# Performance work log

Hardware: AMD Instinct MI355X
Metric: run time of the kernel (lower is better)

Reference implementation:

```python
import jax, jax.numpy as jnp
import numpy as np

EMBED = 2048
HEADS = 16


def setup_inputs() -> dict:
    key = jax.random.key(0)
    ks = jax.random.split(key, 9)
    N, L, E = 4, 2048, EMBED
    inp = {
        "query": jax.random.normal(ks[0], (N, L, E), dtype=jnp.float32),
        "keys": jax.random.normal(ks[1], (N, L, E), dtype=jnp.float32),
        "values": jax.random.normal(ks[2], (N, L, E), dtype=jnp.float32),
        "mask": jax.random.randint(ks[3], (N, L), 0, 2, dtype=jnp.int32),
        # nn.Linear weights, stored torch-style as (out_features, in_features)
        "Wq": jax.random.normal(ks[4], (E, E), dtype=jnp.float32) * (E ** -0.5),
        "Wk": jax.random.normal(ks[5], (E, E), dtype=jnp.float32) * (E ** -0.5),
        "Wv": jax.random.normal(ks[6], (E, E), dtype=jnp.float32) * (E ** -0.5),
        "Wo": jax.random.normal(ks[7], (E, E), dtype=jnp.float32) * (E ** -0.5),
        "bo": jax.random.normal(ks[8], (E,), dtype=jnp.float32) * 0.01,
    }
    return inp


def reference(query, keys, values, mask, Wq, Wk, Wv, Wo, bo):
    N, Lq, E = query.shape
    Lk = keys.shape[1]
    H = HEADS
    D = E // H
    # projections (torch Linear: y = x @ W.T)
    q = (query @ Wq.T).reshape(N, Lq, H, D)   # nqhd
    k = (keys @ Wk.T).reshape(N, Lk, H, D)    # nkhd
    v = (values @ Wv.T).reshape(N, Lk, H, D)  # nkhd
    # attention scores per head: (N, H, Lq, Lk)
    energy = jnp.einsum('nqhd,nkhd->nhqk', q, k)
    # 2D mask (N, Lk): 0 = masked out, broadcast over heads and query positions
    m = mask[:, None, None, :]
    energy = jnp.where(m == 0, jnp.float32(-1e20), energy)
    # source scales by sqrt(embed_size), not sqrt(head_dim)
    attn = jax.nn.softmax(energy * (E ** -0.5), axis=-1)
    out = jnp.einsum('nhqk,nkhd->nqhd', attn, v).reshape(N, Lq, E)
    return out @ Wo.T + bo
```

## Files before the change

kernel.cpp:

```cpp
#include <hip/hip_runtime.h>
#include <stdint.h>


typedef __bf16 bf16;
typedef __bf16 bf16x2 __attribute__((ext_vector_type(2)));
typedef __bf16 bf16x4 __attribute__((ext_vector_type(4)));
typedef __bf16 bf16x8 __attribute__((ext_vector_type(8)));
typedef float  f32x4  __attribute__((ext_vector_type(4)));
typedef uint32_t u32x4 __attribute__((ext_vector_type(4)));

#define MFMA16(a, b, c) __builtin_amdgcn_mfma_f32_16x16x32_bf16(a, b, c, 0, 0, 0)

__device__ __forceinline__ void gload_lds16(const void* g, void* s) {
  __builtin_amdgcn_global_load_lds(
      (const __attribute__((address_space(1))) void*)g,
      (__attribute__((address_space(3))) void*)s, 16, 0, 0);
}

__device__ __forceinline__ uint32_t pkbf(float a, float b) {
  return __builtin_bit_cast(uint32_t, (bf16x2){(bf16)a, (bf16)b});
}

__global__ __launch_bounds__(256) void cvt_bf16(const float* __restrict__ src,
                                                bf16* __restrict__ dst, long n) {
  long i = ((long)blockIdx.x * 256 + threadIdx.x) * 4;
  if (i < n) {
    f32x4 f = *(const f32x4*)(src + i);
    bf16x4 h = { (bf16)f.x, (bf16)f.y, (bf16)f.z, (bf16)f.w };
    *(bf16x4*)(dst + i) = h;
  }
}

__global__ __launch_bounds__(256) void gather_cvt(const float* __restrict__ src,
                                                  bf16* __restrict__ dst,
                                                  const int* __restrict__ idx) {
  long i = (long)blockIdx.x * 256 + threadIdx.x;
  int row = (int)(i >> 8);
  int u = (int)(i & 255);
  int n = row >> 11, p = row & 2047;
  long srow = ((long)n << 11) + idx[(n << 11) + p];
  const float* s = src + srow * 2048 + u * 8;
  f32x4 a = *(const f32x4*)s;
  f32x4 b = *(const f32x4*)(s + 4);
  bf16x8 h = { (bf16)a.x, (bf16)a.y, (bf16)a.z, (bf16)a.w,
               (bf16)b.x, (bf16)b.y, (bf16)b.z, (bf16)b.w };
  *(bf16x8*)(dst + (long)row * 2048 + u * 8) = h;
}

__global__ __launch_bounds__(256) void mask_compact(const int* __restrict__ mask,
                                                    int* __restrict__ idx,
                                                    int* __restrict__ cnts) {
  const int n = blockIdx.x;
  const int t = threadIdx.x, l = t & 63, w = t >> 6;
  const int* m = mask + n * 2048;
  __shared__ int wtot[4];
  int f[8], tt = 0;
  const int base = t * 8;
#pragma unroll
  for (int i = 0; i < 8; ++i) { f[i] = (m[base + i] != 0); tt += f[i]; }
  int sc = tt;
#pragma unroll
  for (int d = 1; d < 64; d <<= 1) {
    int v = __shfl_up(sc, d);
    if (l >= d) sc += v;
  }
  if (l == 63) wtot[w] = sc;
  __syncthreads();
  int woff = 0;
#pragma unroll
  for (int i = 0; i < 4; ++i) if (i < w) woff += wtot[i];
  int off = woff + sc - tt;
#pragma unroll
  for (int i = 0; i < 8; ++i)
    if (f[i]) { idx[n * 2048 + off] = base + i; ++off; }
  int total = wtot[0] + wtot[1] + wtot[2] + wtot[3];
  for (int p = total + t; p < 2048; p += 256) idx[n * 2048 + p] = 2047;
  if (t == 0) { cnts[n] = total; cnts[4 + n] = (total + 127) & ~127; }
}

template <int AEXIT, int OUT_F32, int ADD_BIAS>
__global__ __launch_bounds__(512, 2) void gemm256(const bf16* __restrict__ A,
                                                  const bf16* __restrict__ B,
                                                  void* __restrict__ Cout,
                                                  const float* __restrict__ bias,
                                                  const int* __restrict__ cnts) {
  constexpr int K = 2048, LDC = 2048, NT = 32;
  constexpr int TILE = 256 * 64;
  __shared__ bf16 S[2 * 2 * TILE];
  const int t = threadIdx.x;
  const int l = t & 63, w = t >> 6;
  const int wr = w >> 2, wc = w & 3;
  const int l15 = l & 15, l4 = l >> 4;

  const int Mb = ((blockIdx.x & 7) << 2) + (blockIdx.x >> 3);
  const long tm = (long)Mb * 256;
  const long tn = (long)blockIdx.y * 256;

  if constexpr (AEXIT) {
    int n = (int)(tm >> 11);
    if ((int)(tm & 2047) >= cnts[4 + n]) return;
  }

  const bf16* Ab = A + tm * K;
  const bf16* Bb = B + tn * K;

  auto stage = [&](int T, int p) {
    bf16* sA = S + p * 2 * TILE;
    bf16* sB = sA + TILE;
    const bf16* Ak = Ab + T * 64;
    const bf16* Bk = Bb + T * 64;
#pragma unroll
    for (int i = 0; i < 4; ++i) {
      int u = i * 512 + t;
      int row = u >> 3, slot = u & 7;
      int ss = slot ^ (row & 7);
      gload_lds16(Ak + (long)row * K + ss * 8, sA + u * 8);
    }
#pragma unroll
    for (int i = 0; i < 4; ++i) {
      int u = i * 512 + t;
      int row = u >> 3, slot = u & 7;
      int ss = slot ^ (row & 7);
      gload_lds16(Bk + (long)row * K + ss * 8, sB + u * 8);
    }
  };

  f32x4 acc[8][4];
#pragma unroll
  for (int i = 0; i < 8; ++i)
#pragma unroll
    for (int j = 0; j < 4; ++j) acc[i][j] = (f32x4){0.f, 0.f, 0.f, 0.f};

  stage(0, 0);

  for (int T = 0; T < NT; ++T) {
    const int p = T & 1;
    const bf16* sA = S + p * 2 * TILE;
    const bf16* sB = sA + TILE;

    asm volatile("" ::: "memory");
    __builtin_amdgcn_s_barrier();
    asm volatile("" ::: "memory");
    if (T + 1 < NT) {
      stage(T + 1, p ^ 1);
      asm volatile("s_waitcnt vmcnt(8)" ::: "memory");
    } else {
      asm volatile("s_waitcnt vmcnt(0)" ::: "memory");
    }
    __builtin_amdgcn_s_barrier();
    asm volatile("" ::: "memory");

#pragma unroll
    for (int kk = 0; kk < 2; ++kk) {
      bf16x8 af[8], bf[4];
#pragma unroll
      for (int mi = 0; mi < 8; ++mi) {
        int row = wr * 128 + mi * 16 + l15;
        int slot = (kk * 4 + l4) ^ (row & 7);
        af[mi] = *(const bf16x8*)(sA + row * 64 + slot * 8);
      }
#pragma unroll
      for (int ni = 0; ni < 4; ++ni) {
        int row = wc * 64 + ni * 16 + l15;
        int slot = (kk * 4 + l4) ^ (row & 7);
        bf[ni] = *(const bf16x8*)(sB + row * 64 + slot * 8);
      }
      __builtin_amdgcn_s_setprio(1);
#pragma unroll
      for (int mi = 0; mi < 8; ++mi)
#pragma unroll
        for (int ni = 0; ni < 4; ++ni)
          acc[mi][ni] = MFMA16(af[mi], bf[ni], acc[mi][ni]);
      __builtin_amdgcn_s_setprio(0);
    }
  }

#pragma unroll
  for (int mi = 0; mi < 8; ++mi) {
#pragma unroll
    for (int ni = 0; ni < 4; ++ni) {
      long col = tn + wc * 64 + ni * 16 + l15;
      long row = tm + wr * 128 + mi * 16 + l4 * 4;
#pragma unroll
      for (int r = 0; r < 4; ++r) {
        float v = acc[mi][ni][r];
        if constexpr (OUT_F32) {
          if constexpr (ADD_BIAS) v += bias[col];
          ((float*)Cout)[(row + r) * (long)LDC + col] = v;
        } else {
          ((bf16*)Cout)[(row + r) * (long)LDC + col] = (bf16)v;
        }
      }
    }
  }
}

__global__ __launch_bounds__(512, 4) void attn_fwd(const bf16* __restrict__ Qp,
                                                   const bf16* __restrict__ Kp,
                                                   const bf16* __restrict__ Vp,
                                                   const int* __restrict__ cnts,
                                                   bf16* __restrict__ Op) {
  constexpr int L = 2048, E = 2048, KVB = 64;
  __shared__ bf16 Kt[2][KVB * 128];
  __shared__ bf16 VT[2][128 * KVB];
  const int t = threadIdx.x, l = t & 63, w = t >> 6;
  const int l15 = l & 15, l4 = l >> 4;

  const int b = blockIdx.x;
  const int slot = ((b & 7) << 7) + (b >> 3);
  const int q0 = (slot & 15) << 7;
  const int y = slot >> 4;
  const int n = y >> 4, h = y & 15;
  const int wq = w * 16;
  const float scale = 0.022097086912079608f;

  const bf16* Qb = Qp + ((long)n * L + q0) * E + h * 128;
  const bf16* Kb = Kp + (long)n * L * E + h * 128;
  const bf16* Vb = Vp + (long)n * L * E + h * 128;
  const int cnt = cnts[n];
  const int ntk = (cnt + 63) >> 6;

  bf16x8 qf[4];
#pragma unroll
  for (int kk = 0; kk < 4; ++kk)
    qf[kk] = *(const bf16x8*)(Qb + (long)(wq + l15) * E + kk * 32 + l4 * 8);

  f32x4 o[8];
#pragma unroll
  for (int ni = 0; ni < 8; ++ni) o[ni] = (f32x4){0.f, 0.f, 0.f, 0.f};
  float mreg = -1e20f, lreg = 0.f;

  const int vd0 = (t & 31) * 4;
  const int vj0 = (t >> 5) * 4;

  auto stageK = [&](int kv, int pp) {
#pragma unroll
    for (int i = 0; i < 2; ++i) {
      int u = i * 512 + t;
      int row = u >> 4, sl = u & 15;
      gload_lds16(Kb + (long)(kv + row) * E + ((sl ^ (row & 7)) * 8),
                  &Kt[pp][u * 8]);
    }
  };
  auto loadV = [&](int kv, bf16x4* vr) {
#pragma unroll
    for (int r = 0; r < 4; ++r)
      vr[r] = *(const bf16x4*)(Vb + (long)(kv + vj0 + r) * E + vd0);
  };
  auto writeV = [&](const bf16x4* vr, int pp) {
#pragma unroll
    for (int i = 0; i < 4; ++i) {
      int d = vd0 + i;
      bf16x4 pk = { vr[0][i], vr[1][i], vr[2][i], vr[3][i] };
      *(bf16x4*)(&VT[pp][d * KVB + (vj0 ^ ((d & 7) << 3))]) = pk;
    }
  };

  bf16x4 vr[4];
  stageK(0, 0);
  loadV(0, vr);
  writeV(vr, 0);
  __syncthreads();

  for (int ti = 0; ti < ntk; ++ti) {
    const int p = ti & 1;
    const int kv = ti << 6;
    const bool pre = (ti + 1) < ntk;
    if (pre) {
      stageK(kv + KVB, p ^ 1);
      loadV(kv + KVB, vr);
    }

    f32x4 s[4];
#pragma unroll
    for (int ni = 0; ni < 4; ++ni) s[ni] = (f32x4){0.f, 0.f, 0.f, 0.f};
#pragma unroll
    for (int kk = 0; kk < 4; ++kk) {
      bf16x8 kf[4];
#pragma unroll
      for (int ni = 0; ni < 4; ++ni) {
        int row = ni * 16 + l15;
        int sl = (kk * 4 + l4) ^ (row & 7);
        kf[ni] = *(const bf16x8*)(&Kt[p][row * 128 + sl * 8]);
      }
#pragma unroll
      for (int ni = 0; ni < 4; ++ni)
        s[ni] = MFMA16(kf[ni], qf[kk], s[ni]);
    }

    if (kv + KVB > cnt) {
#pragma unroll
      for (int ni = 0; ni < 4; ++ni)
#pragma unroll
        for (int r = 0; r < 4; ++r) {
          int j = kv + ni * 16 + l4 * 4 + r;
          s[ni][r] = (j < cnt) ? s[ni][r] * scale : -1e20f;
        }
    } else {
#pragma unroll
      for (int ni = 0; ni < 4; ++ni)
#pragma unroll
        for (int r = 0; r < 4; ++r) s[ni][r] *= scale;
    }

    float vmax = -1e20f;
#pragma unroll
    for (int ni = 0; ni < 4; ++ni)
#pragma unroll
      for (int r = 0; r < 4; ++r) vmax = fmaxf(vmax, s[ni][r]);
    vmax = fmaxf(vmax, __shfl_xor(vmax, 16));
    vmax = fmaxf(vmax, __shfl_xor(vmax, 32));
    bool nd = vmax > mreg + 8.0f;
    float corr = nd ? __expf(mreg - vmax) : 1.0f;
    float mn = nd ? vmax : mreg;
    mreg = mn;
    float rsum = 0.f;
    uint32_t u[4][2];
#pragma unroll
    for (int ni = 0; ni < 4; ++ni) {
      float p0 = __expf(s[ni][0] - mn);
      float p1 = __expf(s[ni][1] - mn);
      float p2 = __expf(s[ni][2] - mn);
      float p3 = __expf(s[ni][3] - mn);
      rsum += (p0 + p1) + (p2 + p3);
      u[ni][0] = pkbf(p0, p1);
      u[ni][1] = pkbf(p2, p3);
    }
    rsum += __shfl_xor(rsum, 16);
    rsum += __shfl_xor(rsum, 32);
    lreg = lreg * corr + rsum;
    if (__any(nd)) {
#pragma unroll
      for (int r = 0; r < 4; ++r) {
        float cr = __shfl(corr, l4 * 20 + r);
#pragma unroll
        for (int ni = 0; ni < 8; ++ni) o[ni][r] *= cr;
      }
    }

    const int srcA = l15 + ((l & 16) << 1);
    const int srcB = srcA + 16;
    const bool e5 = (l4 >> 1) != 0;
#pragma unroll
    for (int kk = 0; kk < 2; ++kk) {
      uint32_t a0 = (uint32_t)__shfl((int)u[kk * 2][0], srcA);
      uint32_t a1 = (uint32_t)__shfl((int)u[kk * 2][1], srcA);
      uint32_t a2 = (uint32_t)__shfl((int)u[kk * 2][0], srcB);
      uint32_t a3 = (uint32_t)__shfl((int)u[kk * 2][1], srcB);
      uint32_t b0 = (uint32_t)__shfl((int)u[kk * 2 + 1][0], srcA);
      uint32_t b1 = (uint32_t)__shfl((int)u[kk * 2 + 1][1], srcA);
      uint32_t b2 = (uint32_t)__shfl((int)u[kk * 2 + 1][0], srcB);
      uint32_t b3 = (uint32_t)__shfl((int)u[kk * 2 + 1][1], srcB);
      u32x4 pw = { e5 ? b0 : a0, e5 ? b1 : a1, e5 ? b2 : a2, e5 ? b3 : a3 };
      bf16x8 pa = __builtin_bit_cast(bf16x8, pw);
      bf16x8 vb[8];
#pragma unroll
      for (int ni = 0; ni < 8; ++ni) {
        int d = ni * 16 + l15;
        int col = (kk * 32 + l4 * 8) ^ ((d & 7) << 3);
        vb[ni] = *(const bf16x8*)(&VT[p][d * KVB + col]);
      }
#pragma unroll
      for (int ni = 0; ni < 8; ++ni)
        o[ni] = MFMA16(pa, vb[ni], o[ni]);
    }

    if (pre) writeV(vr, p ^ 1);
    __syncthreads();
  }

  float inv = 1.f / lreg;
#pragma unroll
  for (int r = 0; r < 4; ++r) {
    float iv = __shfl(inv, l4 * 20 + r);
    long grow = (long)n * L + q0 + wq + l4 * 4 + r;
#pragma unroll
    for (int ni = 0; ni < 8; ++ni)
      Op[grow * E + h * 128 + ni * 16 + l15] = (bf16)(o[ni][r] * iv);
  }
}

extern "C" void kernel_launch(void* const* d_in, const int* in_sizes, int n_in,
                              void* d_out, int out_size, void* d_ws, size_t ws_size,
                              hipStream_t stream) {
  (void)in_sizes; (void)n_in; (void)out_size; (void)ws_size;
  const float* query = (const float*)d_in[0];
  const float* keys  = (const float*)d_in[1];
  const float* values= (const float*)d_in[2];
  const int*   mask  = (const int*)d_in[3];
  const float* Wq = (const float*)d_in[4];
  const float* Wk = (const float*)d_in[5];
  const float* Wv = (const float*)d_in[6];
  const float* Wo = (const float*)d_in[7];
  const float* bo = (const float*)d_in[8];
  float* out = (float*)d_out;

  const int N = 4, L = 2048, E = 2048;
  const int M = N * L;
  const long EE = (long)E * E;
  const long ME = (long)M * E;

  int*  idx  = (int*)d_ws;
  int*  cnts = idx + N * 2048;
  bf16* wslot= (bf16*)((char*)d_ws + 65536);
  bf16* xs   = wslot + EE;
  bf16* qp   = xs + ME;
  bf16* kp   = qp + ME;
  bf16* vp   = kp + ME;

  const int cbw = (int)(EE / 4 / 256);
  const int cba = (int)(ME / 4 / 256);
  const int gbl = (int)(ME / 8 / 256);
  dim3 gg(32, 8);

  mask_compact<<<4, 256, 0, stream>>>(mask, idx, cnts);

  cvt_bf16<<<cbw, 256, 0, stream>>>(Wq, wslot, EE);
  cvt_bf16<<<cba, 256, 0, stream>>>(query, xs, ME);
  gemm256<0, 0, 0><<<gg, 512, 0, stream>>>(xs, wslot, qp, nullptr, cnts);

  cvt_bf16<<<cbw, 256, 0, stream>>>(Wk, wslot, EE);
  gather_cvt<<<gbl, 256, 0, stream>>>(keys, xs, idx);
  gemm256<1, 0, 0><<<gg, 512, 0, stream>>>(xs, wslot, kp, nullptr, cnts);

  cvt_bf16<<<cbw, 256, 0, stream>>>(Wv, wslot, EE);
  gather_cvt<<<gbl, 256, 0, stream>>>(values, xs, idx);
  gemm256<1, 0, 0><<<gg, 512, 0, stream>>>(xs, wslot, vp, nullptr, cnts);

  attn_fwd<<<1024, 512, 0, stream>>>(qp, kp, vp, cnts, qp);

  cvt_bf16<<<cbw, 256, 0, stream>>>(Wo, wslot, EE);
  gemm256<0, 1, 1><<<gg, 512, 0, stream>>>(qp, wslot, out, bo, cnts);
}
```

Measured before the change: 478.7 us.

## Batch weight conversions into one launch, remap V loads, raise MFMA priority

Converts all four weight matrices to bf16 in a single launch with separate workspace slots, removing three kernel launches. The activation staging buffer moves into the output buffer, which is free until the final GEMM writes it. Inside attention, the V global-load thread mapping is rearranged and the MFMA blocks are wrapped in s_setprio to favour matrix issue across waves. The separate weight slots use more workspace, and the priority hints and new V mapping may change scheduling in either direction.

```diff
diff --git a/kernel.cpp b/kernel.cpp
--- a/kernel.cpp
+++ b/kernel.cpp
@@ -29,6 +29,23 @@
     bf16x4 h = { (bf16)f.x, (bf16)f.y, (bf16)f.z, (bf16)f.w };
     *(bf16x4*)(dst + i) = h;
   }
+}
+
+__global__ __launch_bounds__(256) void cvt4_bf16(const float* __restrict__ s0,
+                                                 const float* __restrict__ s1,
+                                                 const float* __restrict__ s2,
+                                                 const float* __restrict__ s3,
+                                                 bf16* __restrict__ d0,
+                                                 bf16* __restrict__ d1,
+                                                 bf16* __restrict__ d2,
+                                                 bf16* __restrict__ d3) {
+  int wsel = blockIdx.y;
+  const float* src = wsel == 0 ? s0 : wsel == 1 ? s1 : wsel == 2 ? s2 : s3;
+  bf16* dst = wsel == 0 ? d0 : wsel == 1 ? d1 : wsel == 2 ? d2 : d3;
+  long i = ((long)blockIdx.x * 256 + threadIdx.x) * 4;
+  f32x4 f = *(const f32x4*)(src + i);
+  bf16x4 h = { (bf16)f.x, (bf16)f.y, (bf16)f.z, (bf16)f.w };
+  *(bf16x4*)(dst + i) = h;
 }
 
 __global__ __launch_bounds__(256) void gather_cvt(const float* __restrict__ src,
@@ -230,8 +247,8 @@
   for (int ni = 0; ni < 8; ++ni) o[ni] = (f32x4){0.f, 0.f, 0.f, 0.f};
   float mreg = -1e20f, lreg = 0.f;
 
-  const int vd0 = (t & 31) * 4;
-  const int vj0 = (t >> 5) * 4;
+  const int vj0 = ((l15 & 1) + 2 * l4 + 8 * (w & 1)) * 4;
+  const int vd0 = ((l15 >> 1) + 8 * (w >> 1)) * 4;
 
   auto stageK = [&](int kv, int pp) {
 #pragma unroll
@@ -283,9 +300,11 @@
         int sl = (kk * 4 + l4) ^ (row & 7);
         kf[ni] = *(const bf16x8*)(&Kt[p][row * 128 + sl * 8]);
       }
+      __builtin_amdgcn_s_setprio(1);
 #pragma unroll
       for (int ni = 0; ni < 4; ++ni)
         s[ni] = MFMA16(kf[ni], qf[kk], s[ni]);
+      __builtin_amdgcn_s_setprio(0);
     }
 
     if (kv + KVB > cnt) {
@@ -360,9 +379,11 @@
         int col = (kk * 32 + l4 * 8) ^ ((d & 7) << 3);
         vb[ni] = *(const bf16x8*)(&VT[p][d * KVB + col]);
       }
+      __builtin_amdgcn_s_setprio(1);
 #pragma unroll
       for (int ni = 0; ni < 8; ++ni)
         o[ni] = MFMA16(pa, vb[ni], o[ni]);
+      __builtin_amdgcn_s_setprio(0);
     }
 
     if (pre) writeV(vr, p ^ 1);
@@ -402,11 +423,14 @@
 
   int*  idx  = (int*)d_ws;
   int*  cnts = idx + N * 2048;
-  bf16* wslot= (bf16*)((char*)d_ws + 65536);
-  bf16* xs   = wslot + EE;
-  bf16* qp   = xs + ME;
+  bf16* Wqb  = (bf16*)((char*)d_ws + 65536);
+  bf16* Wkb  = Wqb + EE;
+  bf16* Wvb  = Wkb + EE;
+  bf16* Wob  = Wvb + EE;
+  bf16* qp   = Wob + EE;
   bf16* kp   = qp + ME;
   bf16* vp   = kp + ME;
+  bf16* xs   = (bf16*)d_out;
 
   const int cbw = (int)(EE / 4 / 256);
   const int cba = (int)(ME / 4 / 256);
@@ -414,21 +438,18 @@
   dim3 gg(32, 8);
 
   mask_compact<<<4, 256, 0, stream>>>(mask, idx, cnts);
-
-  cvt_bf16<<<cbw, 256, 0, stream>>>(Wq, wslot, EE);
+  cvt4_bf16<<<dim3(cbw, 4), 256, 0, stream>>>(Wq, Wk, Wv, Wo, Wqb, Wkb, Wvb, Wob);
+
   cvt_bf16<<<cba, 256, 0, stream>>>(query, xs, ME);
-  gemm256<0, 0, 0><<<gg, 512, 0, stream>>>(xs, wslot, qp, nullptr, cnts);
-
-  cvt_bf16<<<cbw, 256, 0, stream>>>(Wk, wslot, EE);
+  gemm256<0, 0, 0><<<gg, 512, 0, stream>>>(xs, Wqb, qp, nullptr, cnts);
+
   gather_cvt<<<gbl, 256, 0, stream>>>(keys, xs, idx);
-  gemm256<1, 0, 0><<<gg, 512, 0, stream>>>(xs, wslot, kp, nullptr, cnts);
-
-  cvt_bf16<<<cbw, 256, 0, stream>>>(Wv, wslot, EE);
+  gemm256<1, 0, 0><<<gg, 512, 0, stream>>>(xs, Wkb, kp, nullptr, cnts);
+
   gather_cvt<<<gbl, 256, 0, stream>>>(values, xs, idx);
-  gemm256<1, 0, 0><<<gg, 512, 0, stream>>>(xs, wslot, vp, nullptr, cnts);
+  gemm256<1, 0, 0><<<gg, 512, 0, stream>>>(xs, Wvb, vp, nullptr, cnts);
 
   attn_fwd<<<1024, 512, 0, stream>>>(qp, kp, vp, cnts, qp);
 
-  cvt_bf16<<<cbw, 256, 0, stream>>>(Wo, wslot, EE);
-  gemm256<0, 1, 1><<<gg, 512, 0, stream>>>(qp, wslot, out, bo, cnts);
-}
+  gemm256<0, 1, 1><<<gg, 512, 0, stream>>>(qp, Wob, out, bo, cnts);
+}
```

New measurement: 452.0 us. -5.6%, faster.
